# Optimization experiments

Measured on AMD Instinct MI355X. Metric: run time of the kernel, lower is better.

The kernel has to match this reference:

```python
import jax, jax.numpy as jnp
import numpy as np

N = 100000      # total nodes (batched graphs)
E = 1200000     # total edges
A = 256         # annotation size (hidden_size_orig)
H = 64          # gnn_h_size
T = 4           # num_edge_types
STEPS = 6       # num_timesteps
B = 64          # number of graphs in the batch
NUM_CLS = 2


def setup_inputs() -> dict:
    key = jax.random.key(0)
    ks = jax.random.split(key, 16)
    annotation = jax.random.normal(ks[0], (N, A), dtype=jnp.float32)
    src = jax.random.randint(ks[1], (E,), 0, N, dtype=jnp.int32)
    dst = jax.random.randint(ks[2], (E,), 0, N, dtype=jnp.int32)
    etypes = jax.random.randint(ks[3], (E,), 0, T, dtype=jnp.int32)
    graph_ids = jnp.sort(jax.random.randint(ks[4], (N,), 0, B, dtype=jnp.int32))

    def lin(k, fan_in, shape):
        return jax.random.normal(k, shape, dtype=jnp.float32) / np.sqrt(fan_in).astype(np.float32)

    params = {
        'reduce_W': lin(ks[5], A, (A, H)),
        'reduce_b': jnp.zeros((H,), jnp.float32),
        'edge_W': lin(ks[6], H, (T, H, H)),      # per-edge-type linear
        'edge_b': jnp.zeros((T, H), jnp.float32),
        'gru_Wi': lin(ks[7], H, (3 * H, H)),     # torch GRUCell layout: r,z,n
        'gru_bi': jnp.zeros((3 * H,), jnp.float32),
        'gru_Wh': lin(ks[8], H, (3 * H, H)),
        'gru_bh': jnp.zeros((3 * H,), jnp.float32),
        'gate_W': lin(ks[9], 2 * H, (2 * H, 1)),
        'gate_b': jnp.zeros((1,), jnp.float32),
        'out_W': lin(ks[10], 2 * H, (2 * H, NUM_CLS)),
        'out_b': jnp.zeros((NUM_CLS,), jnp.float32),
    }
    return dict(annotation=annotation, src=src, dst=dst, etypes=etypes,
                graph_ids=graph_ids, **params)


def reference(annotation, src, dst, etypes, graph_ids,
              reduce_W, reduce_b, edge_W, edge_b,
              gru_Wi, gru_bi, gru_Wh, gru_bh,
              gate_W, gate_b, out_W, out_b):
    # reduce_layer
    h0 = annotation @ reduce_W + reduce_b            # [N, H]

    def step(h, _):
        # per-edge-type linear on all nodes: [T, N, H]
        transformed = jnp.einsum('nh,thk->tnk', h, edge_W) + edge_b[:, None, :]
        msg = transformed[etypes, src]               # [E, H] gather per edge
        a = jax.ops.segment_sum(msg, dst, num_segments=N)  # scatter-add
        # GRUCell(a, h)
        gi = a @ gru_Wi.T + gru_bi
        gh = h @ gru_Wh.T + gru_bh
        i_r, i_z, i_n = jnp.split(gi, 3, axis=-1)
        h_r, h_z, h_n = jnp.split(gh, 3, axis=-1)
        r = jax.nn.sigmoid(i_r + h_r)
        z = jax.nn.sigmoid(i_z + h_z)
        n = jnp.tanh(i_n + r * h_n)
        h_new = (1.0 - z) * n + z * h
        return h_new, None

    h, _ = jax.lax.scan(step, h0, None, length=STEPS)

    feat = jnp.concatenate([h, h0], axis=-1)         # [N, 2H]

    # GlobalAttentionPooling: segment softmax over gate scores, weighted sum
    gate = feat @ gate_W + gate_b                    # [N, 1]
    gmax = jax.ops.segment_max(gate, graph_ids, num_segments=B)
    gmax = jnp.where(jnp.isfinite(gmax), gmax, 0.0)  # guard empty graphs
    e = jnp.exp(gate - gmax[graph_ids])
    denom = jax.ops.segment_sum(e, graph_ids, num_segments=B)
    alpha = e / denom[graph_ids]                     # [N, 1]
    readout = jax.ops.segment_sum(alpha * feat, graph_ids, num_segments=B)  # [B, 2H]

    logits = readout @ out_W + out_b                 # [B, 2]
    return logits
```

## Files before the change

kernel.cpp:

```cpp
#include <hip/hip_runtime.h>
#include <cstdint>
#include <cstddef>

#define N_NODES 100000
#define N_EDGES 1200000
#define ASIZE 256
#define HSIZE 64
#define NTYPES 4
#define NSTEPS 6
#define NGRAPH 64
#define PS 16

static __device__ __forceinline__ float sigmoidf_(float x) { return 1.0f / (1.0f + expf(-x)); }

__global__ void k_count(const int* __restrict__ dst, int* __restrict__ deg) {
    int e = blockIdx.x * 256 + threadIdx.x;
    if (e < N_EDGES) atomicAdd(&deg[dst[e]], 1);
}

__global__ void k_scan1(const int* __restrict__ deg, int* __restrict__ rs, int* __restrict__ part) {
    __shared__ int sh[256];
    int t = threadIdx.x;
    int base = blockIdx.x * 1024 + t * 4;
    int v0 = (base + 0 < N_NODES) ? deg[base + 0] : 0;
    int v1 = (base + 1 < N_NODES) ? deg[base + 1] : 0;
    int v2 = (base + 2 < N_NODES) ? deg[base + 2] : 0;
    int v3 = (base + 3 < N_NODES) ? deg[base + 3] : 0;
    int s = v0 + v1 + v2 + v3;
    sh[t] = s;
    __syncthreads();
    for (int off = 1; off < 256; off <<= 1) {
        int x = (t >= off) ? sh[t - off] : 0;
        __syncthreads();
        sh[t] += x;
        __syncthreads();
    }
    int excl = sh[t] - s;
    if (t == 255) part[blockIdx.x] = sh[255];
    if (base + 0 < N_NODES) rs[base + 0] = excl;
    if (base + 1 < N_NODES) rs[base + 1] = excl + v0;
    if (base + 2 < N_NODES) rs[base + 2] = excl + v0 + v1;
    if (base + 3 < N_NODES) rs[base + 3] = excl + v0 + v1 + v2;
}

__global__ void k_scan2(int* __restrict__ part, int* __restrict__ rs, int nb) {
    if (threadIdx.x == 0 && blockIdx.x == 0) {
        int run = 0;
        for (int i = 0; i < nb; ++i) { int v = part[i]; part[i] = run; run += v; }
        rs[N_NODES] = run;
    }
}

__global__ void k_scan3(int* __restrict__ rs, const int* __restrict__ part) {
    int i = blockIdx.x * 256 + threadIdx.x;
    if (i < N_NODES) rs[i] += part[i >> 10];
}

__global__ void k_fill(const int* __restrict__ src, const int* __restrict__ dst,
                       const int* __restrict__ ety, const int* __restrict__ rs,
                       int* __restrict__ cur, int* __restrict__ colidx) {
    int e = blockIdx.x * 256 + threadIdx.x;
    if (e < N_EDGES) {
        int d = dst[e];
        int pos = rs[d] + atomicAdd(&cur[d], 1);
        colidx[pos] = src[e] * 256 + ety[e] * 64;
    }
}

__global__ void k_prep2(const float* __restrict__ Wh, const float* __restrict__ Bh,
                        const float* __restrict__ eW, const float* __restrict__ eb,
                        const float* __restrict__ Wi, const float* __restrict__ Bi,
                        float* __restrict__ W256, float* __restrict__ b256,
                        float* __restrict__ Wh192, float* __restrict__ bh192,
                        float* __restrict__ WiA, float* __restrict__ biA) {
    int idx = blockIdx.x * 256 + threadIdx.x;
    if (idx < 64 * 256) {
        int k = idx / 256, c = idx % 256;
        W256[idx] = eW[(size_t)(c >> 6) * 4096 + k * 64 + (c & 63)];
    }
    if (idx < 64 * 192) {
        int k = idx / 192, m = idx % 192;
        int j = m / 3, g = m % 3;
        WiA[idx]   = Wi[(g * 64 + j) * 64 + k];
        Wh192[idx] = Wh[(g * 64 + j) * 64 + k];
    }
    if (idx < 256) b256[idx] = eb[idx];
    if (idx < 192) {
        biA[idx]   = Bi[(idx % 3) * 64 + idx / 3];
        bh192[idx] = Bh[(idx % 3) * 64 + idx / 3];
    }
}

__global__ __launch_bounds__(256) void k_gemm(const float* __restrict__ X, int ldx, int K,
                                              const float* __restrict__ W, int ldw,
                                              const float* __restrict__ bias,
                                              float* __restrict__ Y, float* __restrict__ Y2,
                                              int M) {
    __shared__ float sX[128 * 66];
    __shared__ float sW[64 * 64];
    int tid = threadIdx.x;
    int mtile = blockIdx.x * 64;
    int ntile = blockIdx.y * 128;
    int tc4 = (tid & 15) * 4;
    int tr = tid >> 4;
    float4 acc[8];
#pragma unroll
    for (int i = 0; i < 8; ++i) acc[i] = make_float4(0.f, 0.f, 0.f, 0.f);

    int nkc = K >> 6;
    for (int kc = 0; kc < nkc; ++kc) {
        if (kc) __syncthreads();
#pragma unroll
        for (int i = 0; i < 8; ++i) {
            int lin4 = (i * 256 + tid) * 4;
            int nl = lin4 >> 6, kk = lin4 & 63;
            int n = ntile + nl;
            float4 v = make_float4(0.f, 0.f, 0.f, 0.f);
            if (n < N_NODES) v = *(const float4*)(X + (size_t)n * ldx + kc * 64 + kk);
            float* d = sX + nl * 66 + kk;
            d[0] = v.x; d[1] = v.y; d[2] = v.z; d[3] = v.w;
        }
#pragma unroll
        for (int i = 0; i < 4; ++i) {
            int lin4 = (i * 256 + tid) * 4;
            int kk = lin4 >> 6, c = lin4 & 63;
            float4 v = *(const float4*)(W + (size_t)(kc * 64 + kk) * ldw + mtile + c);
            *(float4*)(sW + kk * 64 + c) = v;
        }
        __syncthreads();
        const float* xr = sX + tr * 8 * 66;
        const float* wr = sW + tc4;
        for (int kk = 0; kk < 64; kk += 2) {
            float4 wA = *(const float4*)(wr + kk * 64);
            float4 wB = *(const float4*)(wr + (kk + 1) * 64);
            float xA[8], xB[8];
#pragma unroll
            for (int i = 0; i < 8; ++i) { xA[i] = xr[i * 66 + kk]; xB[i] = xr[i * 66 + kk + 1]; }
#pragma unroll
            for (int i = 0; i < 8; ++i) {
                acc[i].x = fmaf(xA[i], wA.x, acc[i].x);
                acc[i].y = fmaf(xA[i], wA.y, acc[i].y);
                acc[i].z = fmaf(xA[i], wA.z, acc[i].z);
                acc[i].w = fmaf(xA[i], wA.w, acc[i].w);
            }
#pragma unroll
            for (int i = 0; i < 8; ++i) {
                acc[i].x = fmaf(xB[i], wB.x, acc[i].x);
                acc[i].y = fmaf(xB[i], wB.y, acc[i].y);
                acc[i].z = fmaf(xB[i], wB.z, acc[i].z);
                acc[i].w = fmaf(xB[i], wB.w, acc[i].w);
            }
        }
    }
    float4 bv = *(const float4*)(bias + mtile + tc4);
#pragma unroll
    for (int i = 0; i < 8; ++i) {
        int n = ntile + tr * 8 + i;
        if (n < N_NODES) {
            float4 y;
            y.x = acc[i].x + bv.x; y.y = acc[i].y + bv.y;
            y.z = acc[i].z + bv.z; y.w = acc[i].w + bv.w;
            *(float4*)(Y + (size_t)n * M + mtile + tc4) = y;
            if (Y2) *(float4*)(Y2 + (size_t)n * M + mtile + tc4) = y;
        }
    }
}

__global__ __launch_bounds__(256) void k_gemm_red(const float* __restrict__ X,
                                                  const float* __restrict__ W,
                                                  const float* __restrict__ bias,
                                                  float* __restrict__ Y,
                                                  float* __restrict__ Y2) {
    __shared__ float sX[128 * 66];
    __shared__ float sW[64 * 64];
    int tid = threadIdx.x;
    int ntile = blockIdx.x * 128;
    int tc4 = (tid & 15) * 4;
    int tr = tid >> 4;
    int swr = tid >> 4;
    int swc = (tid & 15) * 4;

    float4 acc[8];
#pragma unroll
    for (int i = 0; i < 8; ++i) acc[i] = make_float4(0.f, 0.f, 0.f, 0.f);

    float4 xreg[8];
    float4 wreg[4];
#pragma unroll
    for (int i = 0; i < 8; ++i) {
        int lin4 = (i * 256 + tid) * 4;
        int nl = lin4 >> 6, kk = lin4 & 63;
        int n = ntile + nl;
        float4 v = make_float4(0.f, 0.f, 0.f, 0.f);
        if (n < N_NODES) v = *(const float4*)(X + (size_t)n * 256 + kk);
        xreg[i] = v;
    }
#pragma unroll
    for (int i = 0; i < 4; ++i)
        wreg[i] = *(const float4*)(W + (size_t)(i * 16 + swr) * 64 + swc);

    for (int kc = 0; kc < 4; ++kc) {
#pragma unroll
        for (int i = 0; i < 8; ++i) {
            int lin4 = (i * 256 + tid) * 4;
            int nl = lin4 >> 6, kk = lin4 & 63;
            float* d = sX + nl * 66 + kk;
            d[0] = xreg[i].x; d[1] = xreg[i].y; d[2] = xreg[i].z; d[3] = xreg[i].w;
        }
#pragma unroll
        for (int i = 0; i < 4; ++i)
            *(float4*)(sW + (i * 16 + swr) * 64 + swc) = wreg[i];
        __syncthreads();
        if (kc < 3) {
#pragma unroll
            for (int i = 0; i < 8; ++i) {
                int lin4 = (i * 256 + tid) * 4;
                int nl = lin4 >> 6, kk = lin4 & 63;
                int n = ntile + nl;
                float4 v = make_float4(0.f, 0.f, 0.f, 0.f);
                if (n < N_NODES) v = *(const float4*)(X + (size_t)n * 256 + (kc + 1) * 64 + kk);
                xreg[i] = v;
            }
#pragma unroll
            for (int i = 0; i < 4; ++i)
                wreg[i] = *(const float4*)(W + (size_t)((kc + 1) * 64 + i * 16 + swr) * 64 + swc);
        }
        const float* xr = sX + tr * 8 * 66;
        const float* wrp = sW + tc4;
        for (int kk = 0; kk < 64; kk += 2) {
            float4 wA = *(const float4*)(wrp + kk * 64);
            float4 wB = *(const float4*)(wrp + (kk + 1) * 64);
            float xA[8], xB[8];
#pragma unroll
            for (int i = 0; i < 8; ++i) { xA[i] = xr[i * 66 + kk]; xB[i] = xr[i * 66 + kk + 1]; }
#pragma unroll
            for (int i = 0; i < 8; ++i) {
                acc[i].x = fmaf(xA[i], wA.x, acc[i].x);
                acc[i].y = fmaf(xA[i], wA.y, acc[i].y);
                acc[i].z = fmaf(xA[i], wA.z, acc[i].z);
                acc[i].w = fmaf(xA[i], wA.w, acc[i].w);
            }
#pragma unroll
            for (int i = 0; i < 8; ++i) {
                acc[i].x = fmaf(xB[i], wB.x, acc[i].x);
                acc[i].y = fmaf(xB[i], wB.y, acc[i].y);
                acc[i].z = fmaf(xB[i], wB.z, acc[i].z);
                acc[i].w = fmaf(xB[i], wB.w, acc[i].w);
            }
        }
        if (kc < 3) __syncthreads();
    }
    float4 bv = *(const float4*)(bias + tc4);
#pragma unroll
    for (int i = 0; i < 8; ++i) {
        int n = ntile + tr * 8 + i;
        if (n < N_NODES) {
            float4 y;
            y.x = acc[i].x + bv.x; y.y = acc[i].y + bv.y;
            y.z = acc[i].z + bv.z; y.w = acc[i].w + bv.w;
            *(float4*)(Y + (size_t)n * 64 + tc4) = y;
            *(float4*)(Y2 + (size_t)n * 64 + tc4) = y;
        }
    }
}

__global__ void k_aggregate(const float* __restrict__ buf1, const int* __restrict__ rs,
                            const int* __restrict__ colidx, float* __restrict__ a) {
    int l = threadIdx.x & 63;
    int n = blockIdx.x * 4 + (threadIdx.x >> 6);
    int sub = l >> 4;
    int kq = (l & 15) * 4;
    int beg = rs[n], end = rs[n + 1];
    float4 acc = make_float4(0.f, 0.f, 0.f, 0.f);
    int s = beg;
    for (; s + 15 < end; s += 16) {
        int c0 = colidx[s + sub];
        int c1 = colidx[s + 4 + sub];
        int c2 = colidx[s + 8 + sub];
        int c3 = colidx[s + 12 + sub];
        float4 v0 = *(const float4*)(buf1 + (size_t)c0 + kq);
        float4 v1 = *(const float4*)(buf1 + (size_t)c1 + kq);
        float4 v2 = *(const float4*)(buf1 + (size_t)c2 + kq);
        float4 v3 = *(const float4*)(buf1 + (size_t)c3 + kq);
        acc.x += v0.x; acc.y += v0.y; acc.z += v0.z; acc.w += v0.w;
        acc.x += v1.x; acc.y += v1.y; acc.z += v1.z; acc.w += v1.w;
        acc.x += v2.x; acc.y += v2.y; acc.z += v2.z; acc.w += v2.w;
        acc.x += v3.x; acc.y += v3.y; acc.z += v3.z; acc.w += v3.w;
    }
    for (; s + 3 < end; s += 4) {
        int c = colidx[s + sub];
        float4 v = *(const float4*)(buf1 + (size_t)c + kq);
        acc.x += v.x; acc.y += v.y; acc.z += v.z; acc.w += v.w;
    }
    for (; s < end; ++s) {
        if (sub == 0) {
            int c = colidx[s];
            float4 v = *(const float4*)(buf1 + (size_t)c + kq);
            acc.x += v.x; acc.y += v.y; acc.z += v.z; acc.w += v.w;
        }
    }
    float4 t;
    t.x = acc.x + __shfl_xor(acc.x, 16, 64);
    t.y = acc.y + __shfl_xor(acc.y, 16, 64);
    t.z = acc.z + __shfl_xor(acc.z, 16, 64);
    t.w = acc.w + __shfl_xor(acc.w, 16, 64);
    float4 r;
    r.x = t.x + __shfl_xor(t.x, 32, 64);
    r.y = t.y + __shfl_xor(t.y, 32, 64);
    r.z = t.z + __shfl_xor(t.z, 32, 64);
    r.w = t.w + __shfl_xor(t.w, 32, 64);
    if (sub == 0) *(float4*)(a + (size_t)n * 64 + kq) = r;
}

__global__ __launch_bounds__(256) void k_gruF2(const float* __restrict__ A,
                                               const float* __restrict__ WiA,
                                               const float* __restrict__ biA,
                                               const float* __restrict__ Wh192,
                                               const float* __restrict__ bh192,
                                               float* __restrict__ H) {
    __shared__ float sX[64 * 34];
    __shared__ float sW[32 * 192];
    int tid = threadIdx.x;
    int ntile = blockIdx.x * 64;
    int tc = tid & 15;
    int tr = tid >> 4;
    float acc[2][4][12];
#pragma unroll
    for (int p = 0; p < 2; ++p)
#pragma unroll
        for (int i = 0; i < 4; ++i)
#pragma unroll
            for (int c = 0; c < 12; ++c) acc[p][i][c] = 0.f;

#pragma unroll
    for (int ph = 0; ph < 2; ++ph) {
        const float* Xsrc = (ph == 0) ? A : H;
        const float* Wsrc = (ph == 0) ? WiA : Wh192;
        for (int kc = 0; kc < 2; ++kc) {
            if (ph || kc) __syncthreads();
#pragma unroll
            for (int i = 0; i < 2; ++i) {
                int lin4 = (i * 256 + tid) * 4;
                int nl = lin4 >> 5, kk = lin4 & 31;
                int n = ntile + nl;
                float4 v = make_float4(0.f, 0.f, 0.f, 0.f);
                if (n < N_NODES) v = *(const float4*)(Xsrc + (size_t)n * 64 + kc * 32 + kk);
                float* d = sX + nl * 34 + kk;
                d[0] = v.x; d[1] = v.y; d[2] = v.z; d[3] = v.w;
            }
            {
                int kk = tid >> 3, c = (tid & 7) * 24;
                const float* srcp = Wsrc + (size_t)(kc * 32 + kk) * 192 + c;
                float* d = sW + kk * 192 + c;
#pragma unroll
                for (int u = 0; u < 6; ++u) *(float4*)(d + 4 * u) = *(const float4*)(srcp + 4 * u);
            }
            __syncthreads();
            const float* xr = sX + tr * 4 * 34;
            const float* wr = sW + tc * 12;
            for (int kk = 0; kk < 32; kk += 2) {
                float4 w0 = *(const float4*)(wr + kk * 192);
                float4 w1 = *(const float4*)(wr + kk * 192 + 4);
                float4 w2 = *(const float4*)(wr + kk * 192 + 8);
                float4 u0 = *(const float4*)(wr + (kk + 1) * 192);
                float4 u1 = *(const float4*)(wr + (kk + 1) * 192 + 4);
                float4 u2 = *(const float4*)(wr + (kk + 1) * 192 + 8);
                float xA[4], xB[4];
#pragma unroll
                for (int i = 0; i < 4; ++i) { xA[i] = xr[i * 34 + kk]; xB[i] = xr[i * 34 + kk + 1]; }
#pragma unroll
                for (int i = 0; i < 4; ++i) {
                    acc[ph][i][0]  = fmaf(xA[i], w0.x, acc[ph][i][0]);
                    acc[ph][i][1]  = fmaf(xA[i], w0.y, acc[ph][i][1]);
                    acc[ph][i][2]  = fmaf(xA[i], w0.z, acc[ph][i][2]);
                    acc[ph][i][3]  = fmaf(xA[i], w0.w, acc[ph][i][3]);
                    acc[ph][i][4]  = fmaf(xA[i], w1.x, acc[ph][i][4]);
                    acc[ph][i][5]  = fmaf(xA[i], w1.y, acc[ph][i][5]);
                    acc[ph][i][6]  = fmaf(xA[i], w1.z, acc[ph][i][6]);
                    acc[ph][i][7]  = fmaf(xA[i], w1.w, acc[ph][i][7]);
                    acc[ph][i][8]  = fmaf(xA[i], w2.x, acc[ph][i][8]);
                    acc[ph][i][9]  = fmaf(xA[i], w2.y, acc[ph][i][9]);
                    acc[ph][i][10] = fmaf(xA[i], w2.z, acc[ph][i][10]);
                    acc[ph][i][11] = fmaf(xA[i], w2.w, acc[ph][i][11]);
                }
#pragma unroll
                for (int i = 0; i < 4; ++i) {
                    acc[ph][i][0]  = fmaf(xB[i], u0.x, acc[ph][i][0]);
                    acc[ph][i][1]  = fmaf(xB[i], u0.y, acc[ph][i][1]);
                    acc[ph][i][2]  = fmaf(xB[i], u0.z, acc[ph][i][2]);
                    acc[ph][i][3]  = fmaf(xB[i], u0.w, acc[ph][i][3]);
                    acc[ph][i][4]  = fmaf(xB[i], u1.x, acc[ph][i][4]);
                    acc[ph][i][5]  = fmaf(xB[i], u1.y, acc[ph][i][5]);
                    acc[ph][i][6]  = fmaf(xB[i], u1.z, acc[ph][i][6]);
                    acc[ph][i][7]  = fmaf(xB[i], u1.w, acc[ph][i][7]);
                    acc[ph][i][8]  = fmaf(xB[i], u2.x, acc[ph][i][8]);
                    acc[ph][i][9]  = fmaf(xB[i], u2.y, acc[ph][i][9]);
                    acc[ph][i][10] = fmaf(xB[i], u2.z, acc[ph][i][10]);
                    acc[ph][i][11] = fmaf(xB[i], u2.w, acc[ph][i][11]);
                }
            }
        }
    }
    float bb[12], bh[12];
    {
        float4 b0 = *(const float4*)(biA + tc * 12);
        float4 b1 = *(const float4*)(biA + tc * 12 + 4);
        float4 b2 = *(const float4*)(biA + tc * 12 + 8);
        bb[0] = b0.x; bb[1] = b0.y; bb[2] = b0.z; bb[3] = b0.w;
        bb[4] = b1.x; bb[5] = b1.y; bb[6] = b1.z; bb[7] = b1.w;
        bb[8] = b2.x; bb[9] = b2.y; bb[10] = b2.z; bb[11] = b2.w;
        float4 c0 = *(const float4*)(bh192 + tc * 12);
        float4 c1 = *(const float4*)(bh192 + tc * 12 + 4);
        float4 c2 = *(const float4*)(bh192 + tc * 12 + 8);
        bh[0] = c0.x; bh[1] = c0.y; bh[2] = c0.z; bh[3] = c0.w;
        bh[4] = c1.x; bh[5] = c1.y; bh[6] = c1.z; bh[7] = c1.w;
        bh[8] = c2.x; bh[9] = c2.y; bh[10] = c2.z; bh[11] = c2.w;
    }
#pragma unroll
    for (int i = 0; i < 4; ++i) {
        int n = ntile + tr * 4 + i;
        if (n >= N_NODES) continue;
        float gg[12];
#pragma unroll
        for (int c = 0; c < 12; ++c) gg[c] = acc[1][i][c] + bh[c];
        float4 hv = *(const float4*)(H + (size_t)n * 64 + tc * 4);
        float res[4];
#pragma unroll
        for (int jj = 0; jj < 4; ++jj) {
            int c = jj * 3;
            float r = sigmoidf_(acc[0][i][c] + bb[c] + gg[c]);
            float z = sigmoidf_(acc[0][i][c + 1] + bb[c + 1] + gg[c + 1]);
            float nn = tanhf(acc[0][i][c + 2] + bb[c + 2] + r * gg[c + 2]);
            float hj = (jj == 0) ? hv.x : (jj == 1) ? hv.y : (jj == 2) ? hv.z : hv.w;
            res[jj] = (1.f - z) * nn + z * hj;
        }
        float4 o; o.x = res[0]; o.y = res[1]; o.z = res[2]; o.w = res[3];
        *(float4*)(H + (size_t)n * 64 + tc * 4) = o;
    }
}

__global__ void k_bounds(const int* __restrict__ gid, int* __restrict__ start) {
    int n = blockIdx.x * 256 + threadIdx.x;
    if (n < N_NODES) {
        int g = gid[n];
        if (n == 0) {
            for (int x = 0; x <= g; ++x) start[x] = 0;
        } else {
            int pg = gid[n - 1];
            for (int x = pg + 1; x <= g; ++x) start[x] = n;
        }
        if (n == N_NODES - 1) {
            for (int x = g + 1; x <= NGRAPH; ++x) start[x] = N_NODES;
        }
    }
}

__global__ void k_gate2(const float* __restrict__ H, const float* __restrict__ H0,
                        const float* __restrict__ gW, const float* __restrict__ gb,
                        float* __restrict__ gate) {
    int l = threadIdx.x & 63;
    int n = blockIdx.x * 4 + (threadIdx.x >> 6);
    float v = H[(size_t)n * 64 + l] * gW[l] + H0[(size_t)n * 64 + l] * gW[64 + l];
    for (int off = 32; off > 0; off >>= 1) v += __shfl_xor(v, off, 64);
    if (l == 0) gate[n] = v + gb[0];
}

__global__ __launch_bounds__(64) void k_poolA(const float* __restrict__ gate,
                                              const int* __restrict__ start,
                                              float* __restrict__ pmax) {
    int g = blockIdx.x, s = blockIdx.y;
    int beg = start[g], len = start[g + 1] - beg;
    int sb = beg + (int)((long long)len * s / PS);
    int se = beg + (int)((long long)len * (s + 1) / PS);
    float m = -INFINITY;
    for (int n = sb + threadIdx.x; n < se; n += 64) m = fmaxf(m, gate[n]);
    for (int off = 32; off > 0; off >>= 1) m = fmaxf(m, __shfl_xor(m, off, 64));
    if (threadIdx.x == 0) pmax[g * PS + s] = m;
}

__global__ void k_poolB(const float* __restrict__ pmax, float* __restrict__ gm) {
    int g = threadIdx.x;
    float m = -INFINITY;
    for (int s = 0; s < PS; ++s) m = fmaxf(m, pmax[g * PS + s]);
    if (!isfinite(m)) m = 0.0f;
    gm[g] = m;
}

__global__ __launch_bounds__(256) void k_poolC(const float* __restrict__ H,
                                               const float* __restrict__ H0,
                                               const float* __restrict__ gate,
                                               const int* __restrict__ start,
                                               const float* __restrict__ gm,
                                               float* __restrict__ pnum,
                                               float* __restrict__ pden) {
    int g = blockIdx.x, s = blockIdx.y;
    int beg = start[g], len = start[g + 1] - beg;
    int sb = beg + (int)((long long)len * s / PS);
    int se = beg + (int)((long long)len * (s + 1) / PS);
    int t = threadIdx.x;
    int lane = t & 63, wave = t >> 6;
    float m = gm[g];
    __shared__ float shh[4][64], sh0[4][64], ses[4];
    float ah = 0.f, ah0 = 0.f, es = 0.f;
    for (int n = sb + wave; n < se; n += 4) {
        float e = expf(gate[n] - m);
        es += e;
        ah  += e * H [(size_t)n * 64 + lane];
        ah0 += e * H0[(size_t)n * 64 + lane];
    }
    shh[wave][lane] = ah; sh0[wave][lane] = ah0;
    if (lane == 0) ses[wave] = es;
    __syncthreads();
    if (wave == 0) {
        float r  = shh[0][lane] + shh[1][lane] + shh[2][lane] + shh[3][lane];
        float r0 = sh0[0][lane] + sh0[1][lane] + sh0[2][lane] + sh0[3][lane];
        int base = (g * PS + s) * 128;
        pnum[base + lane]      = r;
        pnum[base + 64 + lane] = r0;
        if (lane == 0) pden[g * PS + s] = ses[0] + ses[1] + ses[2] + ses[3];
    }
}

__global__ __launch_bounds__(128) void k_poolD(const float* __restrict__ pnum,
                                               const float* __restrict__ pden,
                                               float* __restrict__ ro) {
    int g = blockIdx.x;
    int c = threadIdx.x;
    float den = 0.f;
    for (int s = 0; s < PS; ++s) den += pden[g * PS + s];
    float nu = 0.f;
    for (int s = 0; s < PS; ++s) nu += pnum[(g * PS + s) * 128 + c];
    ro[g * 128 + c] = (den > 0.f) ? nu / den : 0.f;
}

__global__ void k_logits(const float* __restrict__ ro, const float* __restrict__ oW,
                         const float* __restrict__ ob, float* __restrict__ out) {
    int t = threadIdx.x;
    int b = t >> 1;
    int c = t & 1;
    float acc = ob[c];
    for (int k = 0; k < 128; ++k) acc = fmaf(ro[b * 128 + k], oW[k * 2 + c], acc);
    out[b * 2 + c] = acc;
}

extern "C" void kernel_launch(void* const* d_in, const int* in_sizes, int n_in,
                              void* d_out, int out_size, void* d_ws, size_t ws_size,
                              hipStream_t stream) {
    (void)in_sizes; (void)n_in; (void)out_size; (void)ws_size;
    const float* ann = (const float*)d_in[0];
    const int* src   = (const int*)d_in[1];
    const int* dst   = (const int*)d_in[2];
    const int* ety   = (const int*)d_in[3];
    const int* gid   = (const int*)d_in[4];
    const float* rW  = (const float*)d_in[5];
    const float* rb  = (const float*)d_in[6];
    const float* eW  = (const float*)d_in[7];
    const float* eb  = (const float*)d_in[8];
    const float* Wi  = (const float*)d_in[9];
    const float* Bi  = (const float*)d_in[10];
    const float* Wh  = (const float*)d_in[11];
    const float* Bh  = (const float*)d_in[12];
    const float* gW  = (const float*)d_in[13];
    const float* gb  = (const float*)d_in[14];
    const float* oW  = (const float*)d_in[15];
    const float* ob  = (const float*)d_in[16];
    float* out = (float*)d_out;

    char* p = (char*)d_ws;
    auto take = [&](size_t nbytes) -> void* {
        void* r = (void*)p;
        p += (nbytes + 255) & ~((size_t)255);
        return r;
    };
    float* h0      = (float*)take((size_t)N_NODES * 64 * 4);
    float* h       = (float*)take((size_t)N_NODES * 64 * 4);
    float* abuf    = (float*)take((size_t)N_NODES * 64 * 4);
    float* buf1    = (float*)take((size_t)N_NODES * 256 * 4);
    float* W256    = (float*)take(64 * 256 * 4);
    float* b256    = (float*)take(256 * 4);
    float* Wh192   = (float*)take(64 * 192 * 4);
    float* bh192   = (float*)take(192 * 4);
    float* WiA     = (float*)take(64 * 192 * 4);
    float* biA     = (float*)take(192 * 4);
    int* deg       = (int*)take((size_t)N_NODES * 4);
    int* cur       = (int*)take((size_t)N_NODES * 4);
    int* rs        = (int*)take((size_t)(N_NODES + 1) * 4);
    int* part      = (int*)take(512);
    int* colidx    = (int*)take((size_t)N_EDGES * 4);
    float* gate    = (float*)take((size_t)N_NODES * 4);
    int* start     = (int*)take((size_t)(NGRAPH + 1) * 4);
    float* pmax    = (float*)take(NGRAPH * PS * 4);
    float* gm      = (float*)take(NGRAPH * 4);
    float* pnum    = (float*)take((size_t)NGRAPH * PS * 128 * 4);
    float* pden    = (float*)take(NGRAPH * PS * 4);
    float* ro      = (float*)take(NGRAPH * 128 * 4);

    hipMemsetAsync(deg, 0, (size_t)N_NODES * 4, stream);
    hipMemsetAsync(cur, 0, (size_t)N_NODES * 4, stream);
    k_count<<<(N_EDGES + 255) / 256, 256, 0, stream>>>(dst, deg);
    int nb = (N_NODES + 1023) / 1024;
    k_scan1<<<nb, 256, 0, stream>>>(deg, rs, part);
    k_scan2<<<1, 64, 0, stream>>>(part, rs, nb);
    k_scan3<<<(N_NODES + 255) / 256, 256, 0, stream>>>(rs, part);
    k_fill<<<(N_EDGES + 255) / 256, 256, 0, stream>>>(src, dst, ety, rs, cur, colidx);

    k_prep2<<<112, 256, 0, stream>>>(Wh, Bh, eW, eb, Wi, Bi, W256, b256, Wh192, bh192, WiA, biA);
    k_bounds<<<(N_NODES + 255) / 256, 256, 0, stream>>>(gid, start);

    int ntiles = (N_NODES + 127) / 128;

    k_gemm_red<<<ntiles, 256, 0, stream>>>(ann, rW, rb, h, h0);

    for (int s = 0; s < NSTEPS; ++s) {
        k_gemm<<<dim3(4, ntiles), 256, 0, stream>>>(h, 64, 64, W256, 256, b256,
                                                    buf1, nullptr, 256);
        k_aggregate<<<N_NODES / 4, 256, 0, stream>>>(buf1, rs, colidx, abuf);
        k_gruF2<<<(N_NODES + 63) / 64, 256, 0, stream>>>(abuf, WiA, biA, Wh192, bh192, h);
    }

    k_gate2<<<N_NODES / 4, 256, 0, stream>>>(h, h0, gW, gb, gate);
    k_poolA<<<dim3(NGRAPH, PS), 64, 0, stream>>>(gate, start, pmax);
    k_poolB<<<1, 64, 0, stream>>>(pmax, gm);
    k_poolC<<<dim3(NGRAPH, PS), 256, 0, stream>>>(h, h0, gate, start, gm, pnum, pden);
    k_poolD<<<NGRAPH, 128, 0, stream>>>(pnum, pden, ro);
    k_logits<<<1, 128, 0, stream>>>(ro, oW, ob, out);
}
```

Baseline: 1.567 ms.

## Fuse next-step edge-type transform into GRU kernel and deepen aggregate unroll

The per-step edge-type GEMM (h times the 64x256 weight) is folded into the GRU kernel's epilogue. The new h tile is kept transposed in shared memory and multiplied by W256 in four 64-column chunks to write buf1 directly, which removes a separate kernel launch and a reread of h on every step but the last. The GRU input staging now uses a transposed shared layout so activations load as float4, and the aggregate loop is unrolled to 32 edges for more loads in flight. The costs are more shared memory per block (about 50KB, which may lower occupancy) and a longer serial epilogue in the GRU kernel.

```diff
diff --git a/kernel.cpp b/kernel.cpp
--- a/kernel.cpp
+++ b/kernel.cpp
@@ -273,19 +273,31 @@
     int beg = rs[n], end = rs[n + 1];
     float4 acc = make_float4(0.f, 0.f, 0.f, 0.f);
     int s = beg;
-    for (; s + 15 < end; s += 16) {
+    for (; s + 31 < end; s += 32) {
         int c0 = colidx[s + sub];
         int c1 = colidx[s + 4 + sub];
         int c2 = colidx[s + 8 + sub];
         int c3 = colidx[s + 12 + sub];
+        int c4 = colidx[s + 16 + sub];
+        int c5 = colidx[s + 20 + sub];
+        int c6 = colidx[s + 24 + sub];
+        int c7 = colidx[s + 28 + sub];
         float4 v0 = *(const float4*)(buf1 + (size_t)c0 + kq);
         float4 v1 = *(const float4*)(buf1 + (size_t)c1 + kq);
         float4 v2 = *(const float4*)(buf1 + (size_t)c2 + kq);
         float4 v3 = *(const float4*)(buf1 + (size_t)c3 + kq);
+        float4 v4 = *(const float4*)(buf1 + (size_t)c4 + kq);
+        float4 v5 = *(const float4*)(buf1 + (size_t)c5 + kq);
+        float4 v6 = *(const float4*)(buf1 + (size_t)c6 + kq);
+        float4 v7 = *(const float4*)(buf1 + (size_t)c7 + kq);
         acc.x += v0.x; acc.y += v0.y; acc.z += v0.z; acc.w += v0.w;
         acc.x += v1.x; acc.y += v1.y; acc.z += v1.z; acc.w += v1.w;
         acc.x += v2.x; acc.y += v2.y; acc.z += v2.z; acc.w += v2.w;
         acc.x += v3.x; acc.y += v3.y; acc.z += v3.z; acc.w += v3.w;
+        acc.x += v4.x; acc.y += v4.y; acc.z += v4.z; acc.w += v4.w;
+        acc.x += v5.x; acc.y += v5.y; acc.z += v5.z; acc.w += v5.w;
+        acc.x += v6.x; acc.y += v6.y; acc.z += v6.z; acc.w += v6.w;
+        acc.x += v7.x; acc.y += v7.y; acc.z += v7.z; acc.w += v7.w;
     }
     for (; s + 3 < end; s += 4) {
         int c = colidx[s + sub];
@@ -312,14 +324,19 @@
     if (sub == 0) *(float4*)(a + (size_t)n * 64 + kq) = r;
 }
 
-__global__ __launch_bounds__(256) void k_gruF2(const float* __restrict__ A,
+__global__ __launch_bounds__(256) void k_gruF3(const float* __restrict__ A,
                                                const float* __restrict__ WiA,
                                                const float* __restrict__ biA,
                                                const float* __restrict__ Wh192,
                                                const float* __restrict__ bh192,
-                                               float* __restrict__ H) {
-    __shared__ float sX[64 * 34];
+                                               const float* __restrict__ W256,
+                                               const float* __restrict__ b256,
+                                               float* __restrict__ H,
+                                               float* __restrict__ buf1,
+                                               int do_trans) {
+    __shared__ float sXT[32 * 68];
     __shared__ float sW[32 * 192];
+    __shared__ float sHT[64 * 68];
     int tid = threadIdx.x;
     int ntile = blockIdx.x * 64;
     int tc = tid & 15;
@@ -340,13 +357,16 @@
             if (ph || kc) __syncthreads();
 #pragma unroll
             for (int i = 0; i < 2; ++i) {
-                int lin4 = (i * 256 + tid) * 4;
-                int nl = lin4 >> 5, kk = lin4 & 31;
+                int lin = i * 256 + tid;
+                int nl = lin >> 3;
+                int kk = (lin & 7) * 4;
                 int n = ntile + nl;
                 float4 v = make_float4(0.f, 0.f, 0.f, 0.f);
                 if (n < N_NODES) v = *(const float4*)(Xsrc + (size_t)n * 64 + kc * 32 + kk);
-                float* d = sX + nl * 34 + kk;
-                d[0] = v.x; d[1] = v.y; d[2] = v.z; d[3] = v.w;
+                sXT[(kk + 0) * 68 + nl] = v.x;
+                sXT[(kk + 1) * 68 + nl] = v.y;
+                sXT[(kk + 2) * 68 + nl] = v.z;
+                sXT[(kk + 3) * 68 + nl] = v.w;
             }
             {
                 int kk = tid >> 3, c = (tid & 7) * 24;
@@ -356,7 +376,6 @@
                 for (int u = 0; u < 6; ++u) *(float4*)(d + 4 * u) = *(const float4*)(srcp + 4 * u);
             }
             __syncthreads();
-            const float* xr = sX + tr * 4 * 34;
             const float* wr = sW + tc * 12;
             for (int kk = 0; kk < 32; kk += 2) {
                 float4 w0 = *(const float4*)(wr + kk * 192);
@@ -365,9 +384,10 @@
                 float4 u0 = *(const float4*)(wr + (kk + 1) * 192);
                 float4 u1 = *(const float4*)(wr + (kk + 1) * 192 + 4);
                 float4 u2 = *(const float4*)(wr + (kk + 1) * 192 + 8);
-                float xA[4], xB[4];
-#pragma unroll
-                for (int i = 0; i < 4; ++i) { xA[i] = xr[i * 34 + kk]; xB[i] = xr[i * 34 + kk + 1]; }
+                float4 xA4 = *(const float4*)(sXT + kk * 68 + tr * 4);
+                float4 xB4 = *(const float4*)(sXT + (kk + 1) * 68 + tr * 4);
+                float xA[4] = {xA4.x, xA4.y, xA4.z, xA4.w};
+                float xB[4] = {xB4.x, xB4.y, xB4.z, xB4.w};
 #pragma unroll
                 for (int i = 0; i < 4; ++i) {
                     acc[ph][i][0]  = fmaf(xA[i], w0.x, acc[ph][i][0]);
@@ -436,6 +456,62 @@
         }
         float4 o; o.x = res[0]; o.y = res[1]; o.z = res[2]; o.w = res[3];
         *(float4*)(H + (size_t)n * 64 + tc * 4) = o;
+        if (do_trans) {
+#pragma unroll
+            for (int jj = 0; jj < 4; ++jj)
+                sHT[(tc * 4 + jj) * 68 + (tr * 4 + i)] = res[jj];
+        }
+    }
+    if (do_trans) {
+        __syncthreads();
+        int tc2 = tc * 4;
+        for (int mt = 0; mt < 4; ++mt) {
+            if (mt) __syncthreads();
+#pragma unroll
+            for (int i = 0; i < 4; ++i) {
+                int idx = i * 256 + tid;
+                int row = idx >> 4, c4 = (idx & 15) * 4;
+                *(float4*)(sW + row * 64 + c4) =
+                    *(const float4*)(W256 + (size_t)row * 256 + mt * 64 + c4);
+            }
+            __syncthreads();
+            float4 tacc[4];
+#pragma unroll
+            for (int i = 0; i < 4; ++i) tacc[i] = make_float4(0.f, 0.f, 0.f, 0.f);
+            for (int kk = 0; kk < 64; kk += 2) {
+                float4 wA = *(const float4*)(sW + kk * 64 + tc2);
+                float4 wB = *(const float4*)(sW + (kk + 1) * 64 + tc2);
+                float4 xA4 = *(const float4*)(sHT + kk * 68 + tr * 4);
+                float4 xB4 = *(const float4*)(sHT + (kk + 1) * 68 + tr * 4);
+                float xA[4] = {xA4.x, xA4.y, xA4.z, xA4.w};
+                float xB[4] = {xB4.x, xB4.y, xB4.z, xB4.w};
+#pragma unroll
+                for (int i = 0; i < 4; ++i) {
+                    tacc[i].x = fmaf(xA[i], wA.x, tacc[i].x);
+                    tacc[i].y = fmaf(xA[i], wA.y, tacc[i].y);
+                    tacc[i].z = fmaf(xA[i], wA.z, tacc[i].z);
+                    tacc[i].w = fmaf(xA[i], wA.w, tacc[i].w);
+                }
+#pragma unroll
+                for (int i = 0; i < 4; ++i) {
+                    tacc[i].x = fmaf(xB[i], wB.x, tacc[i].x);
+                    tacc[i].y = fmaf(xB[i], wB.y, tacc[i].y);
+                    tacc[i].z = fmaf(xB[i], wB.z, tacc[i].z);
+                    tacc[i].w = fmaf(xB[i], wB.w, tacc[i].w);
+                }
+            }
+            float4 bv = *(const float4*)(b256 + mt * 64 + tc2);
+#pragma unroll
+            for (int i = 0; i < 4; ++i) {
+                int n = ntile + tr * 4 + i;
+                if (n < N_NODES) {
+                    float4 y;
+                    y.x = tacc[i].x + bv.x; y.y = tacc[i].y + bv.y;
+                    y.z = tacc[i].z + bv.z; y.w = tacc[i].w + bv.w;
+                    *(float4*)(buf1 + (size_t)n * 256 + mt * 64 + tc2) = y;
+                }
+            }
+        }
     }
 }
 
@@ -611,11 +687,14 @@
 
     k_gemm_red<<<ntiles, 256, 0, stream>>>(ann, rW, rb, h, h0);
 
+    k_gemm<<<dim3(4, ntiles), 256, 0, stream>>>(h, 64, 64, W256, 256, b256,
+                                                buf1, nullptr, 256);
+
     for (int s = 0; s < NSTEPS; ++s) {
-        k_gemm<<<dim3(4, ntiles), 256, 0, stream>>>(h, 64, 64, W256, 256, b256,
-                                                    buf1, nullptr, 256);
         k_aggregate<<<N_NODES / 4, 256, 0, stream>>>(buf1, rs, colidx, abuf);
-        k_gruF2<<<(N_NODES + 63) / 64, 256, 0, stream>>>(abuf, WiA, biA, Wh192, bh192, h);
+        k_gruF3<<<(N_NODES + 63) / 64, 256, 0, stream>>>(abuf, WiA, biA, Wh192, bh192,
+                                                         W256, b256, h, buf1,
+                                                         (s < NSTEPS - 1) ? 1 : 0);
     }
 
     k_gate2<<<N_NODES / 4, 256, 0, stream>>>(h, h0, gW, gb, gate);
```

Result: faster. 1.513 ms (-3.5%).
